# Optimization experiments

Hardware: AMD Instinct MI355X
Metric: run time of the kernel (lower is better)

Reference implementation:

```python
import jax, jax.numpy as jnp
import numpy as np

H = 128
N_EXPERT = 100000
N_TEAM = 50000
N_EDGE = 600000
N_LABEL = 500000


def _sage(x_src, x_dst, src, dst, Wl, Wr, b, n_dst):
    # PyG SAGEConv: lin_l(mean of gathered neighbor feats) + lin_r(x_dst)
    msg = x_src[src]                                   # [E, H] gather
    agg = jax.ops.segment_sum(msg, dst, num_segments=n_dst)      # [n_dst, H]
    cnt = jax.ops.segment_sum(jnp.ones((src.shape[0], 1), x_src.dtype), dst,
                              num_segments=n_dst)      # [n_dst, 1]
    agg = agg / jnp.maximum(cnt, 1.0)
    return agg @ Wl + b + x_dst @ Wr


def setup_inputs() -> dict:
    key = jax.random.key(0)
    ks = jax.random.split(key, 20)
    inp = {
        'x_expert': jax.random.normal(ks[0], (N_EXPERT, H), jnp.float32),
        'x_team': jax.random.normal(ks[1], (N_TEAM, H), jnp.float32),
        'src_expert': jax.random.randint(ks[2], (N_EDGE,), 0, N_EXPERT),
        'dst_team': jax.random.randint(ks[3], (N_EDGE,), 0, N_TEAM),
        'label_src': jax.random.randint(ks[4], (N_LABEL,), 0, N_EXPERT),
        'label_dst': jax.random.randint(ks[5], (N_LABEL,), 0, N_TEAM),
    }
    s = 0.02
    names = ['W1et_l', 'W1et_r', 'W1te_l', 'W1te_r',
             'W2et_l', 'W2et_r', 'W2te_l', 'W2te_r']
    for i, n in enumerate(names):
        inp[n] = s * jax.random.normal(ks[6 + i], (H, H), jnp.float32)
    for i, n in enumerate(['b1et', 'b1te', 'b2et', 'b2te']):
        inp[n] = jnp.zeros((H,), jnp.float32)
    return inp


def reference(x_expert, x_team, src_expert, dst_team, label_src, label_dst,
              W1et_l, W1et_r, W1te_l, W1te_r,
              W2et_l, W2et_r, W2te_l, W2te_r,
              b1et, b1te, b2et, b2te):
    n_e, n_t = x_expert.shape[0], x_team.shape[0]
    # layer 1 (hetero: expert->team and reverse team->expert), ReLU
    h_team = jax.nn.relu(_sage(x_expert, x_team, src_expert, dst_team,
                               W1et_l, W1et_r, b1et, n_t))
    h_expert = jax.nn.relu(_sage(x_team, x_expert, dst_team, src_expert,
                                 W1te_l, W1te_r, b1te, n_e))
    # layer 2, no activation
    z_team = _sage(h_expert, h_team, src_expert, dst_team,
                   W2et_l, W2et_r, b2et, n_t)
    z_expert = _sage(h_team, h_expert, dst_team, src_expert,
                     W2te_l, W2te_r, b2te, n_e)
    # edge dot-product classifier on supervision edges
    return (z_expert[label_src] * z_team[label_dst]).sum(axis=-1)
```

## Files before the change

### kernel.cpp

```cpp
#include <hip/hip_runtime.h>

#define H 128
#define CH 4096
typedef unsigned short ushort_t;
typedef unsigned int uint_t;
typedef unsigned long long u64_t;
using s16x8 = __attribute__((ext_vector_type(8))) short;
using f32x4 = __attribute__((ext_vector_type(4))) float;

__device__ __forceinline__ ushort_t f2bf(float x) {
  uint_t u = __float_as_uint(x);
  return (ushort_t)((u + 0x7fff + ((u >> 16) & 1)) >> 16);
}
__device__ __forceinline__ float bflo(uint_t u) { return __uint_as_float(u << 16); }
__device__ __forceinline__ float bfhi(uint_t u) { return __uint_as_float(u & 0xffff0000u); }

__device__ __forceinline__ void gload_lds16(const void* g, void* l) {
  __builtin_amdgcn_global_load_lds(
      (const __attribute__((address_space(1))) unsigned int*)(unsigned long long)g,
      (__attribute__((address_space(3))) unsigned int*)(unsigned int)(unsigned long long)l,
      16, 0, 0);
}

__global__ __launch_bounds__(256) void prep_kernel(
    const float* __restrict__ xa, const float* __restrict__ xb,
    size_t n4a, size_t n4tot, uint2* __restrict__ xout,
    const float* __restrict__ Wl0, const float* __restrict__ Wr0,
    const float* __restrict__ Wl1, const float* __restrict__ Wr1,
    const float* __restrict__ Wl2, const float* __restrict__ Wr2,
    const float* __restrict__ Wl3, const float* __restrict__ Wr3,
    ushort_t* __restrict__ wdst, int* __restrict__ bcnt, int nbz) {
  const int b = blockIdx.x;
  const int tid = threadIdx.x;
  if (b < 2048) {
    size_t i = (size_t)b * 256 + tid;
    size_t s = 2048 * 256;
    for (; i < n4tot; i += s) {
      float4 v = (i < n4a) ? ((const float4*)xa)[i] : ((const float4*)xb)[i - n4a];
      uint2 r;
      r.x = (uint_t)f2bf(v.x) | ((uint_t)f2bf(v.y) << 16);
      r.y = (uint_t)f2bf(v.z) | ((uint_t)f2bf(v.w) << 16);
      xout[i] = r;
    }
  } else if (b < 2560) {
    int i = (b - 2048) * 256 + tid;
    int w = i >> 15;
    int ii = i & 32767;
    int j = ii & 7;
    int lane = (ii >> 3) & 63;
    int nf = (ii >> 9) & 7;
    int ks = ii >> 12;
    int k = ks * 32 + (lane >> 4) * 8 + j;
    int nn = nf * 16 + (lane & 15);
    const float* Wl = (w == 0) ? Wl0 : (w == 1) ? Wl1 : (w == 2) ? Wl2 : Wl3;
    const float* Wr = (w == 0) ? Wr0 : (w == 1) ? Wr1 : (w == 2) ? Wr2 : Wr3;
    float v = (k < H) ? Wl[k * H + nn] : Wr[(k - H) * H + nn];
    wdst[i] = f2bf(v);
  } else {
    for (int i = tid; i < nbz; i += 256) bcnt[i] = 0;
  }
}

__global__ __launch_bounds__(256) void bucket_count(
    const int* __restrict__ src, const int* __restrict__ dst, const int* __restrict__ ld,
    int* __restrict__ bcnt, int E, int L, int nct, int NBt, int NBe) {
  __shared__ int hist[256];
  const int b = blockIdx.x;
  const int tid = threadIdx.x;
  int stream, i0, n, base, shift;
  if (b < nct) { stream = 0; i0 = b * CH; n = E; base = 0; shift = 8; }
  else if (b < 2 * nct) { stream = 1; i0 = (b - nct) * CH; n = E; base = NBt; shift = 9; }
  else { stream = 2; i0 = (b - 2 * nct) * CH; n = L; base = NBt + NBe; shift = 8; }
  const int* idx = (stream == 0) ? dst : (stream == 1) ? src : ld;
  const int i1 = min(n, i0 + CH);
  hist[tid] = 0;
  __syncthreads();
  for (int i = i0 + tid; i < i1; i += 256) atomicAdd(&hist[idx[i] >> shift], 1);
  __syncthreads();
  int h = hist[tid];
  if (h) atomicAdd(&bcnt[base + tid], h);
}

__global__ void scan_buckets(const int* __restrict__ bcnt, int* __restrict__ boff,
                             int* __restrict__ cur, int n) {
  __shared__ int s[256];
  const int t = threadIdx.x;
  int carry = 0;
  for (int base = 0; base < n; base += 256) {
    int i = base + t;
    int v = (i < n) ? bcnt[i] : 0;
    s[t] = v;
    __syncthreads();
    for (int off = 1; off < 256; off <<= 1) {
      int x = (t >= off) ? s[t - off] : 0;
      __syncthreads();
      s[t] += x;
      __syncthreads();
    }
    if (i < n) { boff[i] = s[t] - v + carry; cur[i] = s[t] - v + carry; }
    __syncthreads();
    carry += s[255];
    __syncthreads();
  }
  if (t == 0) boff[n] = carry;
}

__global__ __launch_bounds__(256) void bucket_scatter(
    const int* __restrict__ src, const int* __restrict__ dst,
    const int* __restrict__ ls, const int* __restrict__ ld,
    int* __restrict__ cur, u64_t* __restrict__ recs,
    int E, int L, int nct, int NBt, int NBe) {
  __shared__ int hist[256];
  __shared__ int start[256];
  const int b = blockIdx.x;
  const int tid = threadIdx.x;
  int stream, i0, n, base;
  if (b < nct) { stream = 0; i0 = b * CH; n = E; base = 0; }
  else if (b < 2 * nct) { stream = 1; i0 = (b - nct) * CH; n = E; base = NBt; }
  else { stream = 2; i0 = (b - 2 * nct) * CH; n = L; base = NBt + NBe; }
  const int i1 = min(n, i0 + CH);

  hist[tid] = 0;
  __syncthreads();
  for (int i = i0 + tid; i < i1; i += 256) {
    int d = (stream == 0) ? dst[i] : (stream == 1) ? src[i] : ld[i];
    int bkt = (stream == 1) ? (d >> 9) : (d >> 8);
    atomicAdd(&hist[bkt], 1);
  }
  __syncthreads();
  int h = hist[tid];
  if (h) start[tid] = atomicAdd(&cur[base + tid], h);
  __syncthreads();
  for (int i = i0 + tid; i < i1; i += 256) {
    u64_t rec;
    int bkt;
    if (stream == 0) {
      int d = dst[i];
      rec = ((u64_t)d << 32) | (uint_t)src[i];
      bkt = d >> 8;
    } else if (stream == 1) {
      int d = src[i];
      rec = ((u64_t)d << 32) | (uint_t)dst[i];
      bkt = d >> 9;
    } else {
      int d = ld[i];
      rec = ((u64_t)d << 40) | ((u64_t)(uint_t)ls[i] << 20) | (uint_t)i;
      bkt = d >> 8;
    }
    int pos = start[bkt] + atomicSub(&hist[bkt], 1) - 1;
    recs[pos] = rec;
  }
}

__global__ __launch_bounds__(256) void place_all(
    const u64_t* __restrict__ recs, const int* __restrict__ boff,
    int* __restrict__ off_t, int* __restrict__ off_e, int* __restrict__ off_l,
    int* __restrict__ adj_t, int* __restrict__ adj_e_m, long long* __restrict__ lpair_m,
    int n_t, int n_e, int NBt, int NBe, int NBl) {
  __shared__ int sh[512];
  __shared__ int tmp[256];
  const int b = blockIdx.x;
  const int tid = threadIdx.x;
  int stream, d0, d1, nmax;
  int* offg;
  if (b < NBt) { stream = 0; d0 = b << 8; d1 = min(n_t, d0 + 256); offg = off_t; nmax = n_t; }
  else if (b < NBt + NBe) { stream = 1; d0 = (b - NBt) << 9; d1 = min(n_e, d0 + 512); offg = off_e; nmax = n_e; }
  else { stream = 2; d0 = (b - NBt - NBe) << 8; d1 = min(n_t, d0 + 256); offg = off_l; nmax = n_t; }
  const int nn = d1 - d0;
  const int rs = boff[b], re = boff[b + 1];

  sh[tid] = 0;
  sh[tid + 256] = 0;
  __syncthreads();
  for (int i = rs + tid; i < re; i += 256) {
    u64_t rec = recs[i];
    int d = (stream == 2) ? (int)(rec >> 40) : (int)(rec >> 32);
    atomicAdd(&sh[d - d0], 1);
  }
  __syncthreads();
  int carry = 0;
  for (int c = 0; c < 2; ++c) {
    int idx = c * 256 + tid;
    int v = sh[idx];
    tmp[tid] = v;
    __syncthreads();
    for (int o = 1; o < 256; o <<= 1) {
      int x = (tid >= o) ? tmp[tid - o] : 0;
      __syncthreads();
      tmp[tid] += x;
      __syncthreads();
    }
    int excl = tmp[tid] - v + carry;
    if (idx < nn) {
      offg[d0 + idx] = rs + excl;
      sh[idx] = rs + excl;
    }
    __syncthreads();
    carry += tmp[255];
    __syncthreads();
  }
  if (tid == 0) {
    bool last = (stream == 0 && b == NBt - 1) ||
                (stream == 1 && b == NBt + NBe - 1) ||
                (stream == 2 && b == NBt + NBe + NBl - 1);
    if (last) offg[nmax] = re;
  }
  __syncthreads();
  if (stream == 0) {
    for (int i = rs + tid; i < re; i += 256) {
      u64_t rec = recs[i];
      int d = (int)(rec >> 32);
      adj_t[atomicAdd(&sh[d - d0], 1)] = (int)rec;
    }
  } else if (stream == 1) {
    for (int i = rs + tid; i < re; i += 256) {
      u64_t rec = recs[i];
      int d = (int)(rec >> 32);
      adj_e_m[atomicAdd(&sh[d - d0], 1)] = (int)rec;
    }
  } else {
    for (int i = rs + tid; i < re; i += 256) {
      u64_t rec = recs[i];
      int d = (int)(rec >> 40);
      int lsv = (int)((rec >> 20) & 0xFFFFF);
      int li = (int)(rec & 0xFFFFF);
      lpair_m[atomicAdd(&sh[d - d0], 1)] = ((long long)lsv << 32) | (uint_t)li;
    }
  }
}

__global__ void pull_mean_dual(
    const ushort_t* __restrict__ featA, const int* __restrict__ offA, const int* __restrict__ adjA,
    ushort_t* __restrict__ outA, int nA,
    const ushort_t* __restrict__ featB, const int* __restrict__ offB, const int* __restrict__ adjB,
    ushort_t* __restrict__ outB, int nB) {
  int gid = blockIdx.x * blockDim.x + threadIdx.x;
  int wave = gid >> 6;
  int lane = gid & 63;
  int nw = (gridDim.x * blockDim.x) >> 6;
  for (int v = wave; v < nA + nB; v += nw) {
    const uint_t* f;
    const int* off;
    const int* adj;
    uint_t* o;
    int vv;
    if (v < nA) {
      f = (const uint_t*)featA; off = offA; adj = adjA; o = (uint_t*)outA; vv = v;
    } else {
      f = (const uint_t*)featB; off = offB; adj = adjB; o = (uint_t*)outB; vv = v - nA;
    }
    int s = off[vv], e = off[vv + 1];
    float axs[8], ays[8];
#pragma unroll
    for (int k = 0; k < 8; ++k) { axs[k] = 0.f; ays[k] = 0.f; }
    int i = s;
    for (; i + 8 <= e; i += 8) {
      uint_t u[8];
#pragma unroll
      for (int k = 0; k < 8; ++k) u[k] = f[(size_t)adj[i + k] * 64 + lane];
#pragma unroll
      for (int k = 0; k < 8; ++k) { axs[k] += bflo(u[k]); ays[k] += bfhi(u[k]); }
    }
    for (; i + 4 <= e; i += 4) {
      uint_t u[4];
#pragma unroll
      for (int k = 0; k < 4; ++k) u[k] = f[(size_t)adj[i + k] * 64 + lane];
#pragma unroll
      for (int k = 0; k < 4; ++k) { axs[k] += bflo(u[k]); ays[k] += bfhi(u[k]); }
    }
    for (; i < e; ++i) {
      uint_t u = f[(size_t)adj[i] * 64 + lane];
      axs[0] += bflo(u); ays[0] += bfhi(u);
    }
    float sx = ((axs[0] + axs[1]) + (axs[2] + axs[3])) + ((axs[4] + axs[5]) + (axs[6] + axs[7]));
    float sy = ((ays[0] + ays[1]) + (ays[2] + ays[3])) + ((ays[4] + ays[5]) + (ays[6] + ays[7]));
    float rd = 1.0f / fmaxf((float)(e - s), 1.0f);
    o[(size_t)vv * 64 + lane] = (uint_t)f2bf(sx * rd) | ((uint_t)f2bf(sy * rd) << 16);
  }
}

template <bool RELU>
__global__ __launch_bounds__(256, 2) void gemm_mfma_dual(
    const ushort_t* __restrict__ aggA, const ushort_t* __restrict__ xdA,
    const ushort_t* __restrict__ wfA, const float* __restrict__ biasA,
    ushort_t* __restrict__ outA, int nA, int gA,
    const ushort_t* __restrict__ aggB, const ushort_t* __restrict__ xdB,
    const ushort_t* __restrict__ wfB, const float* __restrict__ biasB,
    ushort_t* __restrict__ outB, int nB) {
  __shared__ __align__(16) ushort_t sA[64 * 128];
  __shared__ __align__(16) ushort_t sX[64 * 128];
  const ushort_t *agg, *xd, *wfrag;
  const float* bias;
  ushort_t* outp;
  int n, b0, nbl;
  if ((int)blockIdx.x < gA) {
    agg = aggA; xd = xdA; wfrag = wfA; bias = biasA; outp = outA; n = nA;
    b0 = blockIdx.x; nbl = gA;
  } else {
    agg = aggB; xd = xdB; wfrag = wfB; bias = biasB; outp = outB; n = nB;
    b0 = blockIdx.x - gA; nbl = gridDim.x - gA;
  }
  const int t = threadIdx.x;
  const int lane = t & 63;
  const int wid = t >> 6;
  const int mrow = (wid >> 1) * 32;
  const int nhalf = (wid & 1) * 64;

  s16x8 B[8][4];
#pragma unroll
  for (int ks = 0; ks < 8; ++ks)
#pragma unroll
    for (int nfi = 0; nfi < 4; ++nfi)
      B[ks][nfi] = *(const s16x8*)(wfrag + (size_t)(((ks << 3) | ((nhalf >> 4) + nfi)) << 9) + (lane << 3));

  float bv[4];
#pragma unroll
  for (int nfi = 0; nfi < 4; ++nfi) bv[nfi] = bias[nhalf + nfi * 16 + (lane & 15)];

  const int lrow = lane >> 4;
  const int pbyte = (lane & 15) << 4;

  const int ntiles = (n + 63) >> 6;
  for (int tile = b0; tile < ntiles; tile += nbl) {
    const int row0 = tile << 6;
#pragma unroll
    for (int i = 0; i < 8; ++i) {
      int reg = (wid << 3) + i;
      int rr = ((reg & 15) << 2) + lrow;
      int row = row0 + rr;
      row = row < n ? row : n - 1;
      int pp = pbyte ^ ((rr & 7) << 4);
      const ushort_t* srcp = (reg < 16 ? agg : xd) + (size_t)row * H + (pp >> 1);
      ushort_t* ldst = (reg < 16 ? sA : sX) + ((reg & 15) << 9);
      gload_lds16(srcp, ldst);
    }
    __syncthreads();

    f32x4 acc[2][4];
#pragma unroll
    for (int mi = 0; mi < 2; ++mi)
#pragma unroll
      for (int nfi = 0; nfi < 4; ++nfi) {
        f32x4 c = {bv[nfi], bv[nfi], bv[nfi], bv[nfi]};
        acc[mi][nfi] = c;
      }

    const int rr0 = mrow + (lane & 15);
    const int rr1 = rr0 + 16;
    const int kx = (lane >> 4) << 4;
    const int sw = (rr0 & 7) << 4;
#pragma unroll
    for (int ks = 0; ks < 8; ++ks) {
      const ushort_t* base = (ks < 4) ? sA : sX;
      const int kb = (ks & 3) << 6;
      s16x8 a0 = *(const s16x8*)((const char*)base + rr0 * 256 + ((kb | kx) ^ sw));
      s16x8 a1 = *(const s16x8*)((const char*)base + rr1 * 256 + ((kb | kx) ^ sw));
#pragma unroll
      for (int nfi = 0; nfi < 4; ++nfi) {
        acc[0][nfi] = __builtin_amdgcn_mfma_f32_16x16x32_bf16(a0, B[ks][nfi], acc[0][nfi], 0, 0, 0);
        acc[1][nfi] = __builtin_amdgcn_mfma_f32_16x16x32_bf16(a1, B[ks][nfi], acc[1][nfi], 0, 0, 0);
      }
    }

#pragma unroll
    for (int mi = 0; mi < 2; ++mi) {
      int rbase = row0 + mrow + mi * 16 + ((lane >> 4) << 2);
#pragma unroll
      for (int r = 0; r < 4; ++r) {
        int row = rbase + r;
        if (row < n) {
#pragma unroll
          for (int nfi = 0; nfi < 4; ++nfi) {
            float v = acc[mi][nfi][r];
            if (RELU) v = fmaxf(v, 0.f);
            outp[(size_t)row * H + nhalf + nfi * 16 + (lane & 15)] = f2bf(v);
          }
        }
      }
    }
    __syncthreads();
  }
}

__global__ void edge_dot_grouped(const ushort_t* __restrict__ ze, const ushort_t* __restrict__ zt,
                                 const int* __restrict__ loff, const long long* __restrict__ lpair,
                                 float* __restrict__ out, int n_t) {
  int gid = blockIdx.x * blockDim.x + threadIdx.x;
  int wave = gid >> 6;
  int lane = gid & 63;
  int nw = (gridDim.x * blockDim.x) >> 6;
  const uint_t* fz = (const uint_t*)ze;
  const uint_t* ft = (const uint_t*)zt;
  for (int v = wave; v < n_t; v += nw) {
    int s = loff[v], e = loff[v + 1];
    if (s == e) continue;
    uint_t ub = ft[(size_t)v * 64 + lane];
    float blo = bflo(ub), bhi = bfhi(ub);
    int i = s;
    for (; i + 4 <= e; i += 4) {
      long long q0 = lpair[i], q1 = lpair[i + 1], q2 = lpair[i + 2], q3 = lpair[i + 3];
      uint_t u0 = fz[(size_t)(int)(q0 >> 32) * 64 + lane];
      uint_t u1 = fz[(size_t)(int)(q1 >> 32) * 64 + lane];
      uint_t u2 = fz[(size_t)(int)(q2 >> 32) * 64 + lane];
      uint_t u3 = fz[(size_t)(int)(q3 >> 32) * 64 + lane];
      float p0 = bflo(u0) * blo + bfhi(u0) * bhi;
      float p1 = bflo(u1) * blo + bfhi(u1) * bhi;
      float p2 = bflo(u2) * blo + bfhi(u2) * bhi;
      float p3 = bflo(u3) * blo + bfhi(u3) * bhi;
#pragma unroll
      for (int o = 32; o; o >>= 1) {
        p0 += __shfl_down(p0, o);
        p1 += __shfl_down(p1, o);
        p2 += __shfl_down(p2, o);
        p3 += __shfl_down(p3, o);
      }
      if (lane == 0) {
        __builtin_nontemporal_store(p0, &out[(int)q0]);
        __builtin_nontemporal_store(p1, &out[(int)q1]);
        __builtin_nontemporal_store(p2, &out[(int)q2]);
        __builtin_nontemporal_store(p3, &out[(int)q3]);
      }
    }
    for (; i < e; ++i) {
      long long q0 = lpair[i];
      uint_t u0 = fz[(size_t)(int)(q0 >> 32) * 64 + lane];
      float p0 = bflo(u0) * blo + bfhi(u0) * bhi;
#pragma unroll
      for (int o = 32; o; o >>= 1) p0 += __shfl_down(p0, o);
      if (lane == 0) __builtin_nontemporal_store(p0, &out[(int)q0]);
    }
  }
}

extern "C" void kernel_launch(void* const* d_in, const int* in_sizes, int n_in,
                              void* d_out, int out_size, void* d_ws, size_t ws_size,
                              hipStream_t stream) {
  const float* x_e = (const float*)d_in[0];
  const float* x_t = (const float*)d_in[1];
  const int* src = (const int*)d_in[2];
  const int* dst = (const int*)d_in[3];
  const int* ls = (const int*)d_in[4];
  const int* ld = (const int*)d_in[5];
  const float* W1et_l = (const float*)d_in[6];
  const float* W1et_r = (const float*)d_in[7];
  const float* W1te_l = (const float*)d_in[8];
  const float* W1te_r = (const float*)d_in[9];
  const float* W2et_l = (const float*)d_in[10];
  const float* W2et_r = (const float*)d_in[11];
  const float* W2te_l = (const float*)d_in[12];
  const float* W2te_r = (const float*)d_in[13];
  const float* b1et = (const float*)d_in[14];
  const float* b1te = (const float*)d_in[15];
  const float* b2et = (const float*)d_in[16];
  const float* b2te = (const float*)d_in[17];

  const int n_e = in_sizes[0] / H;
  const int n_t = in_sizes[1] / H;
  const int E = in_sizes[2];
  const int L = in_sizes[4];
  float* out = (float*)d_out;

  const size_t fe = (size_t)n_e * H;
  const size_t ft = (size_t)n_t * H;
  ushort_t* us = (ushort_t*)d_ws;
  ushort_t* xb_e = us;
  ushort_t* xb_t = xb_e + fe;
  ushort_t* agg_e = xb_t + ft;
  ushort_t* agg_t = agg_e + fe;
  ushort_t* h_e = agg_t + ft;
  ushort_t* h_t = h_e + fe;
  ushort_t* wfrag = h_t + ft;
  int* ib = (int*)(wfrag + 4 * 32768);

  const int Mt = n_t + 1, Me = n_e + 1, Ml = n_t + 1;
  const int NBt = (n_t + 255) >> 8;
  const int NBe = (n_e + 511) >> 9;
  const int NBl = NBt;
  const int NBtot = NBt + NBe + NBl;

  int* off = ib;
  int* bcnt = off + Mt + Me + Ml;
  int* boff = bcnt + NBtot + 1;
  int* cur = boff + NBtot + 1;
  int* adj_t = cur + NBtot;
  int* adj_e = adj_t + E;
  long long* lpair = (long long*)(((unsigned long long)(adj_e + E) + 7) & ~7ULL);
  u64_t* recs = (u64_t*)(lpair + L);

  int* off_t = off;
  int* off_e = off + Mt;
  int* off_l = off + Mt + Me;
  int* adj_e_m = adj_e - E;
  long long* lpair_m = lpair - 2 * (size_t)E;

  const int nct = (E + CH - 1) / CH;
  const int ncl = (L + CH - 1) / CH;

  const dim3 blk(256);

  prep_kernel<<<2561, blk, 0, stream>>>(x_e, x_t, fe / 4, (fe + ft) / 4, (uint2*)xb_e,
                                        W1et_l, W1et_r, W1te_l, W1te_r,
                                        W2et_l, W2et_r, W2te_l, W2te_r,
                                        wfrag, bcnt, NBtot + 1);

  bucket_count<<<2 * nct + ncl, blk, 0, stream>>>(src, dst, ld, bcnt, E, L, nct, NBt, NBe);
  scan_buckets<<<1, blk, 0, stream>>>(bcnt, boff, cur, NBtot);
  bucket_scatter<<<2 * nct + ncl, blk, 0, stream>>>(src, dst, ls, ld, cur, recs,
                                                    E, L, nct, NBt, NBe);
  place_all<<<NBtot, blk, 0, stream>>>(recs, boff, off_t, off_e, off_l,
                                       adj_t, adj_e_m, lpair_m, n_t, n_e, NBt, NBe, NBl);

  const int gt = (n_t + 63) / 64, ge = (n_e + 63) / 64;
  const int gA = min(gt, 512), gB = min(ge, 512);
  const int npull = ((n_t + n_e) + 3) / 4;

  pull_mean_dual<<<npull, blk, 0, stream>>>(xb_e, off_t, adj_t, agg_t, n_t,
                                            xb_t, off_e, adj_e_m, agg_e, n_e);
  gemm_mfma_dual<true><<<gA + gB, blk, 0, stream>>>(
      agg_t, xb_t, wfrag + 0 * 32768, b1et, h_t, n_t, gA,
      agg_e, xb_e, wfrag + 1 * 32768, b1te, h_e, n_e);

  pull_mean_dual<<<npull, blk, 0, stream>>>(h_e, off_t, adj_t, agg_t, n_t,
                                            h_t, off_e, adj_e_m, agg_e, n_e);
  gemm_mfma_dual<false><<<gA + gB, blk, 0, stream>>>(
      agg_t, h_t, wfrag + 2 * 32768, b2et, agg_t, n_t, gA,
      agg_e, h_e, wfrag + 3 * 32768, b2te, agg_e, n_e);

  edge_dot_grouped<<<(n_t + 3) / 4, blk, 0, stream>>>(agg_e, agg_t, off_l, lpair_m, out, n_t);
}
```

Before: 286.5 us.

## Switch intermediates to fp16, vectorize gather and dot kernels with fdot2

Intermediate features and weights change from bf16 to fp16, so packing uses cvt_pkrtz and the GEMM uses the f16 MFMA. The mean-aggregation and edge-dot kernels now let each quarter-wave read a full 16-byte row chunk, so four neighbors are gathered per iteration, and they accumulate with fdot2 instructions before a cross-slot shuffle reduction. The GEMM launch bound is raised to 3 blocks per CU and its grid is fixed at 256/512 blocks. fp16 has a narrower range than bf16, and the hardcoded grid sizes assume the node counts.

```diff
diff --git a/kernel.cpp b/kernel.cpp
--- a/kernel.cpp
+++ b/kernel.cpp
@@ -7,13 +7,14 @@
 typedef unsigned long long u64_t;
 using s16x8 = __attribute__((ext_vector_type(8))) short;
 using f32x4 = __attribute__((ext_vector_type(4))) float;
-
-__device__ __forceinline__ ushort_t f2bf(float x) {
-  uint_t u = __float_as_uint(x);
-  return (ushort_t)((u + 0x7fff + ((u >> 16) & 1)) >> 16);
-}
-__device__ __forceinline__ float bflo(uint_t u) { return __uint_as_float(u << 16); }
-__device__ __forceinline__ float bfhi(uint_t u) { return __uint_as_float(u & 0xffff0000u); }
+using h2 = __attribute__((ext_vector_type(2))) _Float16;
+
+__device__ __forceinline__ float dot2(uint_t a, uint_t b, float c) {
+  return __builtin_amdgcn_fdot2(__builtin_bit_cast(h2, a), __builtin_bit_cast(h2, b), c, false);
+}
+__device__ __forceinline__ uint_t pkh(float a, float b) {
+  return __builtin_bit_cast(uint_t, __builtin_amdgcn_cvt_pkrtz(a, b));
+}
 
 __device__ __forceinline__ void gload_lds16(const void* g, void* l) {
   __builtin_amdgcn_global_load_lds(
@@ -38,8 +39,8 @@
     for (; i < n4tot; i += s) {
       float4 v = (i < n4a) ? ((const float4*)xa)[i] : ((const float4*)xb)[i - n4a];
       uint2 r;
-      r.x = (uint_t)f2bf(v.x) | ((uint_t)f2bf(v.y) << 16);
-      r.y = (uint_t)f2bf(v.z) | ((uint_t)f2bf(v.w) << 16);
+      r.x = pkh(v.x, v.y);
+      r.y = pkh(v.z, v.w);
       xout[i] = r;
     }
   } else if (b < 2560) {
@@ -55,7 +56,7 @@
     const float* Wl = (w == 0) ? Wl0 : (w == 1) ? Wl1 : (w == 2) ? Wl2 : Wl3;
     const float* Wr = (w == 0) ? Wr0 : (w == 1) ? Wr1 : (w == 2) ? Wr2 : Wr3;
     float v = (k < H) ? Wl[k * H + nn] : Wr[(k - H) * H + nn];
-    wdst[i] = f2bf(v);
+    wdst[i] = __builtin_bit_cast(ushort_t, (_Float16)v);
   } else {
     for (int i = tid; i < nbz; i += 256) bcnt[i] = 0;
   }
@@ -237,50 +238,56 @@
   int gid = blockIdx.x * blockDim.x + threadIdx.x;
   int wave = gid >> 6;
   int lane = gid & 63;
+  int slot = lane >> 4;
+  int sl = lane & 15;
   int nw = (gridDim.x * blockDim.x) >> 6;
   for (int v = wave; v < nA + nB; v += nw) {
-    const uint_t* f;
+    const uint4* f;
     const int* off;
     const int* adj;
-    uint_t* o;
+    uint4* o;
     int vv;
     if (v < nA) {
-      f = (const uint_t*)featA; off = offA; adj = adjA; o = (uint_t*)outA; vv = v;
+      f = (const uint4*)featA; off = offA; adj = adjA; o = (uint4*)outA; vv = v;
     } else {
-      f = (const uint_t*)featB; off = offB; adj = adjB; o = (uint_t*)outB; vv = v - nA;
+      f = (const uint4*)featB; off = offB; adj = adjB; o = (uint4*)outB; vv = v - nA;
     }
     int s = off[vv], e = off[vv + 1];
-    float axs[8], ays[8];
-#pragma unroll
-    for (int k = 0; k < 8; ++k) { axs[k] = 0.f; ays[k] = 0.f; }
-    int i = s;
-    for (; i + 8 <= e; i += 8) {
-      uint_t u[8];
-#pragma unroll
-      for (int k = 0; k < 8; ++k) u[k] = f[(size_t)adj[i + k] * 64 + lane];
-#pragma unroll
-      for (int k = 0; k < 8; ++k) { axs[k] += bflo(u[k]); ays[k] += bfhi(u[k]); }
-    }
-    for (; i + 4 <= e; i += 4) {
-      uint_t u[4];
-#pragma unroll
-      for (int k = 0; k < 4; ++k) u[k] = f[(size_t)adj[i + k] * 64 + lane];
-#pragma unroll
-      for (int k = 0; k < 4; ++k) { axs[k] += bflo(u[k]); ays[k] += bfhi(u[k]); }
-    }
-    for (; i < e; ++i) {
-      uint_t u = f[(size_t)adj[i] * 64 + lane];
-      axs[0] += bflo(u); ays[0] += bfhi(u);
-    }
-    float sx = ((axs[0] + axs[1]) + (axs[2] + axs[3])) + ((axs[4] + axs[5]) + (axs[6] + axs[7]));
-    float sy = ((ays[0] + ays[1]) + (ays[2] + ays[3])) + ((ays[4] + ays[5]) + (ays[6] + ays[7]));
-    float rd = 1.0f / fmaxf((float)(e - s), 1.0f);
-    o[(size_t)vv * 64 + lane] = (uint_t)f2bf(sx * rd) | ((uint_t)f2bf(sy * rd) << 16);
+    float acc[8];
+#pragma unroll
+    for (int c = 0; c < 8; ++c) acc[c] = 0.f;
+#pragma unroll 2
+    for (int i = s; i < e; i += 4) {
+      int j = i + slot;
+      bool val = j < e;
+      int idx = adj[val ? j : i];
+      uint4 u = f[(size_t)idx * 16 + sl];
+      uint_t s_lo = val ? 0x00003C00u : 0u;
+      uint_t s_hi = val ? 0x3C000000u : 0u;
+      acc[0] = dot2(u.x, s_lo, acc[0]); acc[1] = dot2(u.x, s_hi, acc[1]);
+      acc[2] = dot2(u.y, s_lo, acc[2]); acc[3] = dot2(u.y, s_hi, acc[3]);
+      acc[4] = dot2(u.z, s_lo, acc[4]); acc[5] = dot2(u.z, s_hi, acc[5]);
+      acc[6] = dot2(u.w, s_lo, acc[6]); acc[7] = dot2(u.w, s_hi, acc[7]);
+    }
+#pragma unroll
+    for (int c = 0; c < 8; ++c) {
+      acc[c] += __shfl_xor(acc[c], 16);
+      acc[c] += __shfl_xor(acc[c], 32);
+    }
+    if (slot == 0) {
+      float rd = 1.0f / fmaxf((float)(e - s), 1.0f);
+      uint4 ov;
+      ov.x = pkh(acc[0] * rd, acc[1] * rd);
+      ov.y = pkh(acc[2] * rd, acc[3] * rd);
+      ov.z = pkh(acc[4] * rd, acc[5] * rd);
+      ov.w = pkh(acc[6] * rd, acc[7] * rd);
+      o[(size_t)vv * 16 + sl] = ov;
+    }
   }
 }
 
 template <bool RELU>
-__global__ __launch_bounds__(256, 2) void gemm_mfma_dual(
+__global__ __launch_bounds__(256, 3) void gemm_mfma_dual(
     const ushort_t* __restrict__ aggA, const ushort_t* __restrict__ xdA,
     const ushort_t* __restrict__ wfA, const float* __restrict__ biasA,
     ushort_t* __restrict__ outA, int nA, int gA,
@@ -357,8 +364,8 @@
       s16x8 a1 = *(const s16x8*)((const char*)base + rr1 * 256 + ((kb | kx) ^ sw));
 #pragma unroll
       for (int nfi = 0; nfi < 4; ++nfi) {
-        acc[0][nfi] = __builtin_amdgcn_mfma_f32_16x16x32_bf16(a0, B[ks][nfi], acc[0][nfi], 0, 0, 0);
-        acc[1][nfi] = __builtin_amdgcn_mfma_f32_16x16x32_bf16(a1, B[ks][nfi], acc[1][nfi], 0, 0, 0);
+        acc[0][nfi] = __builtin_amdgcn_mfma_f32_16x16x32_f16(a0, B[ks][nfi], acc[0][nfi], 0, 0, 0);
+        acc[1][nfi] = __builtin_amdgcn_mfma_f32_16x16x32_f16(a1, B[ks][nfi], acc[1][nfi], 0, 0, 0);
       }
     }
 
@@ -373,7 +380,8 @@
           for (int nfi = 0; nfi < 4; ++nfi) {
             float v = acc[mi][nfi][r];
             if (RELU) v = fmaxf(v, 0.f);
-            outp[(size_t)row * H + nhalf + nfi * 16 + (lane & 15)] = f2bf(v);
+            outp[(size_t)row * H + nhalf + nfi * 16 + (lane & 15)] =
+                __builtin_bit_cast(ushort_t, (_Float16)v);
           }
         }
       }
@@ -388,46 +396,27 @@
   int gid = blockIdx.x * blockDim.x + threadIdx.x;
   int wave = gid >> 6;
   int lane = gid & 63;
+  int slot = lane >> 4;
+  int sl = lane & 15;
   int nw = (gridDim.x * blockDim.x) >> 6;
-  const uint_t* fz = (const uint_t*)ze;
-  const uint_t* ft = (const uint_t*)zt;
+  const uint4* fz = (const uint4*)ze;
+  const uint4* ft = (const uint4*)zt;
   for (int v = wave; v < n_t; v += nw) {
     int s = loff[v], e = loff[v + 1];
     if (s == e) continue;
-    uint_t ub = ft[(size_t)v * 64 + lane];
-    float blo = bflo(ub), bhi = bfhi(ub);
-    int i = s;
-    for (; i + 4 <= e; i += 4) {
-      long long q0 = lpair[i], q1 = lpair[i + 1], q2 = lpair[i + 2], q3 = lpair[i + 3];
-      uint_t u0 = fz[(size_t)(int)(q0 >> 32) * 64 + lane];
-      uint_t u1 = fz[(size_t)(int)(q1 >> 32) * 64 + lane];
-      uint_t u2 = fz[(size_t)(int)(q2 >> 32) * 64 + lane];
-      uint_t u3 = fz[(size_t)(int)(q3 >> 32) * 64 + lane];
-      float p0 = bflo(u0) * blo + bfhi(u0) * bhi;
-      float p1 = bflo(u1) * blo + bfhi(u1) * bhi;
-      float p2 = bflo(u2) * blo + bfhi(u2) * bhi;
-      float p3 = bflo(u3) * blo + bfhi(u3) * bhi;
-#pragma unroll
-      for (int o = 32; o; o >>= 1) {
-        p0 += __shfl_down(p0, o);
-        p1 += __shfl_down(p1, o);
-        p2 += __shfl_down(p2, o);
-        p3 += __shfl_down(p3, o);
-      }
-      if (lane == 0) {
-        __builtin_nontemporal_store(p0, &out[(int)q0]);
-        __builtin_nontemporal_store(p1, &out[(int)q1]);
-        __builtin_nontemporal_store(p2, &out[(int)q2]);
-        __builtin_nontemporal_store(p3, &out[(int)q3]);
-      }
-    }
-    for (; i < e; ++i) {
-      long long q0 = lpair[i];
-      uint_t u0 = fz[(size_t)(int)(q0 >> 32) * 64 + lane];
-      float p0 = bflo(u0) * blo + bfhi(u0) * bhi;
-#pragma unroll
-      for (int o = 32; o; o >>= 1) p0 += __shfl_down(p0, o);
-      if (lane == 0) __builtin_nontemporal_store(p0, &out[(int)q0]);
+    uint4 b = ft[(size_t)v * 16 + sl];
+    for (int i = s; i < e; i += 4) {
+      int j = i + slot;
+      bool val = j < e;
+      long long q = lpair[val ? j : i];
+      int row = (int)(q >> 32);
+      uint4 u = fz[(size_t)row * 16 + sl];
+      float p = dot2(u.x, b.x, dot2(u.y, b.y, dot2(u.z, b.z, dot2(u.w, b.w, 0.f))));
+      p += __shfl_xor(p, 1);
+      p += __shfl_xor(p, 2);
+      p += __shfl_xor(p, 4);
+      p += __shfl_xor(p, 8);
+      if (sl == 0 && val) __builtin_nontemporal_store(p, &out[(int)q]);
     }
   }
 }
@@ -510,8 +499,7 @@
   place_all<<<NBtot, blk, 0, stream>>>(recs, boff, off_t, off_e, off_l,
                                        adj_t, adj_e_m, lpair_m, n_t, n_e, NBt, NBe, NBl);
 
-  const int gt = (n_t + 63) / 64, ge = (n_e + 63) / 64;
-  const int gA = min(gt, 512), gB = min(ge, 512);
+  const int gA = 256, gB = 512;
   const int npull = ((n_t + n_e) + 3) / 4;
 
   pull_mean_dual<<<npull, blk, 0, stream>>>(xb_e, off_t, adj_t, agg_t, n_t,
```

Result: slower. 314.5 us (+9.8%).
